# Kernel optimization log

Hardware: AMD Instinct MI355X
Metric: run time of the kernel (lower is better)

Reference implementation:

```python
import jax, jax.numpy as jnp
import numpy as np

B = 1024      # batchsz
T = 80        # max_review_len
E = 100       # embedding_len
U = 256       # units
V = 10000     # total_words


def _lstm_cell(x, c, h, wf, bf, wi, bi, wc, bc, wo, bo):
    # Faithful to LSTMlayer.call: four separate concat+matmul+bias gates.
    hx = jnp.concatenate([h, x], axis=1)          # [B, U + sec_dim]
    gf = jax.nn.sigmoid(hx @ wf + bf)             # forget gate
    gi = jax.nn.sigmoid(hx @ wi + bi)             # input gate (gr / wr1)
    ct = jnp.tanh(hx @ wc + bc)                   # candidate (wr2)
    c_new = gf * c + gi * ct
    go = jax.nn.sigmoid(hx @ wo + bo)             # output gate
    h_new = go * jnp.tanh(c_new)
    return c_new, h_new


def setup_inputs() -> dict:
    key = jax.random.key(0)
    ks = jax.random.split(key, 21)
    inp = {"tokens": jax.random.randint(ks[0], (B, T), 0, V, dtype=jnp.int32)}
    inp["emb"] = jax.random.normal(ks[1], (V, E), dtype=jnp.float32) * 0.1
    # Layer 1: sec_dim = E; Layer 2: sec_dim = U. stddev=0.1 matches init_weights.
    names = ["wf1", "wi1", "wc1", "wo1", "wf2", "wi2", "wc2", "wo2"]
    dims = [U + E] * 4 + [U + U] * 4
    for i, (n, d) in enumerate(zip(names, dims)):
        inp[n] = jax.random.normal(ks[2 + i], (d, U), dtype=jnp.float32) * 0.1
        inp["b" + n[1:]] = jnp.zeros((U,), dtype=jnp.float32)
    inp["w_out"] = jax.random.normal(ks[10], (U, 1), dtype=jnp.float32) * 0.1
    inp["b_out"] = jnp.zeros((1,), dtype=jnp.float32)
    return inp


def reference(tokens, emb, wf1, bf1, wi1, bi1, wc1, bc1, wo1, bo1,
              wf2, bf2, wi2, bi2, wc2, bc2, wo2, bo2, w_out, b_out):
    x = emb[tokens]                               # [B, T, E]
    init = (jnp.zeros((B, U), x.dtype), jnp.zeros((B, U), x.dtype),
            jnp.zeros((B, U), x.dtype), jnp.zeros((B, U), x.dtype))

    def step(carry, xt):
        c1, h1, c2, h2 = carry
        c1, h1 = _lstm_cell(xt, c1, h1, wf1, bf1, wi1, bi1, wc1, bc1, wo1, bo1)
        c2, h2 = _lstm_cell(h1, c2, h2, wf2, bf2, wi2, bi2, wc2, bc2, wo2, bo2)
        return (c1, h1, c2, h2), None

    carry, _ = jax.lax.scan(step, init, jnp.swapaxes(x, 0, 1))  # scan over T
    h2_last = carry[3]                            # [B, U]
    return jax.nn.sigmoid(h2_last @ w_out + b_out)  # [B, 1]
```

## Files before the change

### kernel.cpp

```cpp
#include <hip/hip_runtime.h>

typedef unsigned short u16;
typedef unsigned int uint;

using f32x4 = __attribute__((ext_vector_type(4))) float;
using bf16x8 = __attribute__((ext_vector_type(8))) __bf16;
using u32x4 = __attribute__((ext_vector_type(4))) uint;

static __device__ __forceinline__ bf16x8 as_bf16x8(uint4 u) {
    union { uint4 a; bf16x8 b; } c; c.a = u; return c.b;
}
static __device__ __forceinline__ bf16x8 as_bf16x8v(u32x4 u) {
    union { u32x4 a; bf16x8 b; } c; c.a = u; return c.b;
}
static __device__ __forceinline__ float bf2f(u16 h) {
    union { uint u; float f; } c; c.u = ((uint)h) << 16; return c.f;
}
static __device__ __forceinline__ u16 f2bf(float f) {
    union { float f; uint u; } c; c.f = f;
    uint u = c.u;
    return (u16)((u + 0x7fffu + ((u >> 16) & 1u)) >> 16);
}
static __device__ __forceinline__ float fast_sigmoid(float x) {
    x = fminf(30.f, fmaxf(-30.f, x));
    return __builtin_amdgcn_rcpf(1.0f + __builtin_amdgcn_exp2f(x * -1.44269504f));
}
static __device__ __forceinline__ float fast_tanh(float x) {
    x = fminf(15.f, fmaxf(-15.f, x));
    return 1.0f - 2.0f * __builtin_amdgcn_rcpf(1.0f + __builtin_amdgcn_exp2f(x * 2.88539008f));
}

static __device__ __forceinline__ u32x4 load_b128_sc0(const u16* p) {
    u32x4 r;
    asm volatile("global_load_dwordx4 %0, %1, off sc0" : "=v"(r) : "v"(p) : "memory");
    return r;
}
static __device__ __forceinline__ void wait_vm0_fence_sched() {
    asm volatile("s_waitcnt vmcnt(0)" ::: "memory");
    __builtin_amdgcn_sched_barrier(0);
}

static __device__ __forceinline__ float vext(f32x4 v, int i) {
    float r = v[0];
    r = (i == 1) ? v[1] : r;
    r = (i == 2) ? v[2] : r;
    r = (i == 3) ? v[3] : r;
    return r;
}
static __device__ __forceinline__ float sel4(float a0, float a1, float a2, float a3, int i) {
    float r = a0;
    r = (i == 1) ? a1 : r;
    r = (i == 2) ? a2 : r;
    r = (i == 3) ? a3 : r;
    return r;
}

static __device__ __forceinline__ int detect_fp32(const uint* w, int nwords) {
    int hits = 0;
    for (int i = 0; i < nwords; ++i) { uint e = (w[i] >> 7) & 0xffu; hits += (e >= 0x80u); }
    return hits > (nwords >> 3);
}
static __device__ __forceinline__ u16 load_bf(const void* p, int i, int fp32) {
    return fp32 ? f2bf(((const float*)p)[i]) : ((const u16*)p)[i];
}

__global__ void pack_w(const void* wf, const void* wi, const void* wc, const void* wo,
                       const void* bbf, const void* bbi, const void* bbc, const void* bbo,
                       u16* __restrict__ wp, u16* __restrict__ bp, int K, int KSTEPS) {
    __shared__ int sfp;
    if (threadIdx.x == 0) sfp = detect_fp32((const uint*)wf, 256);
    __syncthreads();
    const int fp32 = sfp;
    int w = blockIdx.x / KSTEPS, ks = blockIdx.x % KSTEPS;
    int nt = threadIdx.x >> 6, lane = threadIdx.x & 63;
    int c16 = lane & 15, q = lane >> 4;
    int n = w * 64 + nt * 16 + c16;
    int u = n >> 2, g = n & 3;
    const void* W = (g == 0) ? wf : (g == 1) ? wi : (g == 2) ? wc : wo;
    union { u16 v[8]; uint4 u4; } tmp;
#pragma unroll
    for (int j = 0; j < 8; ++j) {
        int k = ks * 32 + q * 8 + j;
        tmp.v[j] = (k < K) ? load_bf(W, k * 256 + u, fp32) : (u16)0;
    }
    *(uint4*)(wp + ((w * KSTEPS + ks) * 4 + nt) * 512 + lane * 8) = tmp.u4;
    if (ks == 0 && threadIdx.x < 64) {
        int n2 = w * 64 + threadIdx.x;
        int g2 = n2 & 3;
        const void* B = (g2 == 0) ? bbf : (g2 == 1) ? bbi : (g2 == 2) ? bbc : bbo;
        bp[n2] = load_bf(B, n2 >> 2, fp32);
    }
}

__global__ void pack_misc(const void* emb, const void* w_out, const void* b_out,
                          u16* __restrict__ embp, u16* __restrict__ wob,
                          u16* __restrict__ bob, uint* __restrict__ hzero) {
    __shared__ int sfp;
    if (threadIdx.x == 0) sfp = detect_fp32((const uint*)emb, 256);
    __syncthreads();
    const int fp32 = sfp;
    int gid = blockIdx.x * blockDim.x + threadIdx.x;
    int stride = gridDim.x * blockDim.x;
    for (int i = gid; i < 1000000; i += stride)
        embp[i] = load_bf(emb, i, fp32);
    for (int i = gid; i < 526336; i += stride) hzero[i] = 0;
    if (blockIdx.x == 0) {
        __shared__ int sfp2;
        if (threadIdx.x == 0) sfp2 = detect_fp32((const uint*)w_out, 128);
        __syncthreads();
        if (threadIdx.x < 256) wob[threadIdx.x] = load_bf(w_out, threadIdx.x, sfp2);
        if (threadIdx.x == 0) bob[0] = load_bf(b_out, 0, sfp2);
    }
}

static __device__ __forceinline__ void wv_wait(uint* grp, uint phase, int lane) {
    const uint* fp = grp + (lane & 15);
    uint* cnt = grp + 32;
    int k = 0;
    while (true) {
        uint v;
        asm volatile("global_load_dword %0, %1, off sc0\n\t"
                     "s_waitcnt vmcnt(0)"
                     : "=v"(v) : "v"(fp) : "memory");
        if (__all((int)(v >= phase))) break;
        if (((++k) & 7) == 0 &&
            __hip_atomic_load(cnt, __ATOMIC_RELAXED,
                              __HIP_MEMORY_SCOPE_AGENT) >= 16u * phase)
            break;
    }
}

static __device__ __forceinline__ void wv_arrive(uint* ldsc_ch, uint* grp, int g,
                                                 uint phase, int lane) {
    asm volatile("s_waitcnt vmcnt(0)" ::: "memory");
    if (lane == 0) {
        uint old = __hip_atomic_fetch_add(ldsc_ch, 1u, __ATOMIC_RELAXED,
                                          __HIP_MEMORY_SCOPE_WORKGROUP);
        if (old == 8u * phase - 1u) {
            uint* slot = grp + g;
            asm volatile("global_store_dword %0, %1, off sc0"
                         :: "v"(slot), "v"(phase) : "memory");
            __hip_atomic_fetch_add(grp + 32, 1u, __ATOMIC_RELAXED,
                                   __HIP_MEMORY_SCOPE_AGENT);
        }
    }
}

#define CSLAB 16384

__global__ void __launch_bounds__(1024, 1)
lstm_kernel(const int* __restrict__ tokens, const u16* __restrict__ embp,
            const u16* __restrict__ wp1, const u16* __restrict__ b1p,
            const u16* __restrict__ wp2, const u16* __restrict__ b2p,
            const u16* __restrict__ wob, const u16* __restrict__ bob,
            u16* __restrict__ h1g, u16* __restrict__ h2g,
            uint* __restrict__ flags, float* __restrict__ out) {
    __shared__ __align__(16) u16 w1s[12 * 4 * 512];
    __shared__ __align__(16) u16 w2s[16 * 4 * 512];
    __shared__ uint ldsc[2];
    __shared__ __align__(16) float outscr[1024];

    const int tid = threadIdx.x;
    const int bid = blockIdx.x;
    const int r2 = bid & 7;
    const int g = bid >> 3;
    const int lane = tid & 63;
    const int wv = tid >> 6;
    const int half = wv >> 3;
    const int w8 = wv & 7;
    const int nt = w8 & 3;
    const int mb = (w8 >> 2) * 2;
    const int c16 = lane & 15, q = lane >> 4;

    const int b = lane & 3;
    const int ulz = nt * 4 + ((lane & 15) >> 2);
    const int gunit = g * 16 + ulz;

    {
        const uint4* s1 = (const uint4*)(wp1 + g * (12 * 4 * 512));
        uint4* d1 = (uint4*)w1s;
        for (int i = tid; i < 3072; i += 1024) d1[i] = s1[i];
        const uint4* s2 = (const uint4*)(wp2 + g * (16 * 4 * 512));
        uint4* d2 = (uint4*)w2s;
        for (int i = tid; i < 4096; i += 1024) d2[i] = s2[i];
        if (tid < 2) ldsc[tid] = 0u;
    }
    ushort4 bl1 = *(const ushort4*)(b1p + gunit * 4);
    ushort4 bl2 = *(const ushort4*)(b2p + gunit * 4);
    const float b1f = bf2f(bl1.x), b1i = bf2f(bl1.y), b1c = bf2f(bl1.z), b1o = bf2f(bl1.w);
    const float b2f = bf2f(bl2.x), b2i = bf2f(bl2.y), b2c = bf2f(bl2.z), b2o = bf2f(bl2.w);
    float c1a = 0.f, c1b = 0.f, c2a = 0.f, c2b = 0.f;
    uint* fg = flags + (half * 8 + r2) * 64;
    uint* lc = &ldsc[half];
    __syncthreads();

    const u16* bp1 = w1s + nt * 512 + lane * 8;
    const u16* bp2 = w2s + nt * 512 + lane * 8;

    ushort4 xlo[4], xhi[4];
#define LOAD_X(m, t)                                                           \
    {                                                                          \
        int row = r2 * 128 + half * 64 + (m) * 16 + c16;                       \
        int tok = tokens[row * 80 + (t)];                                      \
        const u16* xb = embp + tok * 100 + q * 8;                              \
        _Pragma("unroll")                                                      \
        for (int k2 = 0; k2 < 4; ++k2) {                                       \
            xlo[k2] = *(const ushort4*)(xb + k2 * 32);                         \
            xhi[k2] = *(const ushort4*)(xb + k2 * 32 + 4);                     \
        }                                                                      \
    }
#define XFRAG(k2) ({ union { ushort4 a[2]; bf16x8 v; } xu;                     \
                     xu.a[0] = xlo[k2]; xu.a[1] = xhi[k2]; xu.v; })

#define GATES(accv, B0, B1, B2, B3, cref, hout)                                \
    {                                                                          \
        float v0 = vext(accv, b);                                              \
        float v1 = __shfl_xor(vext(accv, b ^ 1), 1, 64);                       \
        float v2 = __shfl_xor(vext(accv, b ^ 2), 2, 64);                       \
        float v3 = __shfl_xor(vext(accv, b ^ 3), 3, 64);                       \
        float zf = sel4(v0, v1, v2, v3, b);                                    \
        float zi = sel4(v0, v1, v2, v3, b ^ 1);                                \
        float zc = sel4(v0, v1, v2, v3, b ^ 2);                                \
        float zo = sel4(v0, v1, v2, v3, b ^ 3);                                \
        float gf = fast_sigmoid(zf + B0);                                      \
        float gi = fast_sigmoid(zi + B1);                                      \
        float gc = fast_tanh(zc + B2);                                         \
        float go = fast_sigmoid(zo + B3);                                      \
        float cn = gf * cref + gi * gc;                                        \
        cref = cn;                                                             \
        hout = f2bf(go * fast_tanh(cn));                                       \
    }

#define MSUB(m, acc1, c1ref, c2ref, p2r, p1r, p2w, p1w, iw)                    \
    {                                                                          \
        const int loffm = (q >> 1) * 1024 + ((m) * 16 + c16) * 16 + (q & 1) * 8; \
        const int hidxm = g * 1024 + ((m) * 16 + q * 4 + b) * 16 + ulz;        \
        const u16* h2b = h2g + (((p2r) * 2 + half) * 8 + r2) * CSLAB + loffm;  \
        const u16* h1b = h1g + (((p1r) * 2 + half) * 8 + r2) * CSLAB + loffm;  \
        u32x4 ag2[8], ag1[8];                                                  \
        _Pragma("unroll")                                                      \
        for (int ks = 0; ks < 8; ++ks) ag2[ks] = load_b128_sc0(h2b + ks * 2048); \
        _Pragma("unroll")                                                      \
        for (int ks = 0; ks < 8; ++ks) ag1[ks] = load_b128_sc0(h1b + ks * 2048); \
        wait_vm0_fence_sched();                                                \
        f32x4 acc2 = (f32x4){0.f, 0.f, 0.f, 0.f};                              \
        _Pragma("unroll")                                                      \
        for (int ks = 0; ks < 8; ++ks)                                         \
            acc2 = __builtin_amdgcn_mfma_f32_16x16x32_bf16(                    \
                as_bf16x8v(ag2[ks]), as_bf16x8(*(const uint4*)(bp2 + ks * 2048)), acc2, 0, 0, 0); \
        _Pragma("unroll")                                                      \
        for (int ks = 0; ks < 8; ++ks)                                         \
            acc2 = __builtin_amdgcn_mfma_f32_16x16x32_bf16(                    \
                as_bf16x8v(ag1[ks]), as_bf16x8(*(const uint4*)(bp2 + (8 + ks) * 2048)), acc2, 0, 0, 0); \
        _Pragma("unroll")                                                      \
        for (int ks = 0; ks < 8; ++ks)                                         \
            acc1 = __builtin_amdgcn_mfma_f32_16x16x32_bf16(                    \
                as_bf16x8v(ag1[ks]), as_bf16x8(*(const uint4*)(bp1 + ks * 2048)), acc1, 0, 0, 0); \
        u16 h2o, h1o;                                                          \
        GATES(acc2, b2f, b2i, b2c, b2o, c2ref, h2o);                           \
        GATES(acc1, b1f, b1i, b1c, b1o, c1ref, h1o);                           \
        h2g[(((p2w) * 2 + half) * 8 + r2) * CSLAB + hidxm] = h2o;              \
        h1g[(((p1w) * 2 + half) * 8 + r2) * CSLAB + hidxm] = h1o;              \
        (void)(iw);                                                            \
    }

    {
        LOAD_X(mb, 0);
        f32x4 acc = (f32x4){0.f, 0.f, 0.f, 0.f};
#pragma unroll
        for (int k2 = 0; k2 < 4; ++k2)
            acc = __builtin_amdgcn_mfma_f32_16x16x32_bf16(
                XFRAG(k2), as_bf16x8(*(const uint4*)(bp1 + (8 + k2) * 2048)), acc, 0, 0, 0);
        u16 h1o;
        GATES(acc, b1f, b1i, b1c, b1o, c1a, h1o);
        h1g[((0 * 2 + half) * 8 + r2) * CSLAB + g * 1024 + (mb * 16 + q * 4 + b) * 16 + ulz] = h1o;
        LOAD_X(mb + 1, 0);
        f32x4 accB = (f32x4){0.f, 0.f, 0.f, 0.f};
#pragma unroll
        for (int k2 = 0; k2 < 4; ++k2)
            accB = __builtin_amdgcn_mfma_f32_16x16x32_bf16(
                XFRAG(k2), as_bf16x8(*(const uint4*)(bp1 + (8 + k2) * 2048)), accB, 0, 0, 0);
        u16 h1oB;
        GATES(accB, b1f, b1i, b1c, b1o, c1b, h1oB);
        h1g[((0 * 2 + half) * 8 + r2) * CSLAB + g * 1024 + ((mb + 1) * 16 + q * 4 + b) * 16 + ulz] = h1oB;
        wv_arrive(lc, fg, g, 1u, lane);
    }

#pragma unroll 1
    for (int i = 0; i < 79; ++i) {
        const int p_h2r = (i + 1) & 1, p_h1r = i & 1;
        const int p_h2w = i & 1, p_h1w = (i + 1) & 1;

        LOAD_X(mb, i + 1);
        f32x4 acc1a = (f32x4){0.f, 0.f, 0.f, 0.f};
#pragma unroll
        for (int k2 = 0; k2 < 4; ++k2)
            acc1a = __builtin_amdgcn_mfma_f32_16x16x32_bf16(
                XFRAG(k2), as_bf16x8(*(const uint4*)(bp1 + (8 + k2) * 2048)), acc1a, 0, 0, 0);
        LOAD_X(mb + 1, i + 1);
        f32x4 acc1b = (f32x4){0.f, 0.f, 0.f, 0.f};
#pragma unroll
        for (int k2 = 0; k2 < 4; ++k2)
            acc1b = __builtin_amdgcn_mfma_f32_16x16x32_bf16(
                XFRAG(k2), as_bf16x8(*(const uint4*)(bp1 + (8 + k2) * 2048)), acc1b, 0, 0, 0);

        wv_wait(fg, (uint)(i + 1), lane);

        MSUB(mb, acc1a, c1a, c2a, p_h2r, p_h1r, p_h2w, p_h1w, i);
        MSUB(mb + 1, acc1b, c1b, c2b, p_h2r, p_h1r, p_h2w, p_h1w, i);

        wv_arrive(lc, fg, g, (uint)(i + 2), lane);
    }

    {
        wv_wait(fg, 80u, lane);
#pragma unroll 1
        for (int s = 0; s < 2; ++s) {
            const int m = mb + s;
            const int loffm = (q >> 1) * 1024 + (m * 16 + c16) * 16 + (q & 1) * 8;
            const int hidxm = g * 1024 + (m * 16 + q * 4 + b) * 16 + ulz;
            const u16* h2b = h2g + ((0 * 2 + half) * 8 + r2) * CSLAB + loffm;
            const u16* h1b = h1g + ((1 * 2 + half) * 8 + r2) * CSLAB + loffm;
            u32x4 ag2[8], ag1[8];
#pragma unroll
            for (int ks = 0; ks < 8; ++ks) ag2[ks] = load_b128_sc0(h2b + ks * 2048);
#pragma unroll
            for (int ks = 0; ks < 8; ++ks) ag1[ks] = load_b128_sc0(h1b + ks * 2048);
            wait_vm0_fence_sched();
            f32x4 acc2 = (f32x4){0.f, 0.f, 0.f, 0.f};
#pragma unroll
            for (int ks = 0; ks < 8; ++ks)
                acc2 = __builtin_amdgcn_mfma_f32_16x16x32_bf16(
                    as_bf16x8v(ag2[ks]), as_bf16x8(*(const uint4*)(bp2 + ks * 2048)), acc2, 0, 0, 0);
#pragma unroll
            for (int ks = 0; ks < 8; ++ks)
                acc2 = __builtin_amdgcn_mfma_f32_16x16x32_bf16(
                    as_bf16x8v(ag1[ks]), as_bf16x8(*(const uint4*)(bp2 + (8 + ks) * 2048)), acc2, 0, 0, 0);
            u16 h2o;
            if (s == 0) { GATES(acc2, b2f, b2i, b2c, b2o, c2a, h2o); }
            else        { GATES(acc2, b2f, b2i, b2c, b2o, c2b, h2o); }
            h2g[((1 * 2 + half) * 8 + r2) * CSLAB + hidxm] = h2o;
        }
        wv_arrive(lc, fg, g, 81u, lane);
        wv_wait(fg, 81u, lane);
    }
    __syncthreads();

    if (g == 0) {
#pragma unroll 1
        for (int ch = 0; ch < 2; ++ch) {
            const u16* base = h2g + ((1 * 2 + ch) * 8 + r2) * CSLAB;
            int rr = tid >> 4, s = tid & 15;
            const u16* hp = base + s * 1024 + rr * 16;
            u32x4 hv0 = load_b128_sc0(hp);
            u32x4 hv1 = load_b128_sc0(hp + 8);
            wait_vm0_fence_sched();
            const u16* wq = wob + s * 16;
            union { u32x4 v[2]; u16 h[16]; } hu; hu.v[0] = hv0; hu.v[1] = hv1;
            float dot = 0.f;
#pragma unroll
            for (int k = 0; k < 16; ++k) dot += bf2f(hu.h[k]) * bf2f(wq[k]);
            __syncthreads();
            outscr[rr * 16 + s] = dot;
            __syncthreads();
            if (tid < 64) {
                float ssum = 0.f;
                for (int k = 0; k < 16; ++k) ssum += outscr[tid * 16 + k];
                out[r2 * 128 + ch * 64 + tid] = fast_sigmoid(ssum + bf2f(bob[0]));
            }
        }
    }
}

extern "C" void kernel_launch(void* const* d_in, const int* in_sizes, int n_in,
                              void* d_out, int out_size, void* d_ws, size_t ws_size,
                              hipStream_t stream) {
    const int* tokens = (const int*)d_in[0];
    const void* emb = d_in[1];
    const void* wf1 = d_in[2];  const void* bf1_ = d_in[3];
    const void* wi1 = d_in[4];  const void* bi1_ = d_in[5];
    const void* wc1 = d_in[6];  const void* bc1_ = d_in[7];
    const void* wo1 = d_in[8];  const void* bo1_ = d_in[9];
    const void* wf2 = d_in[10]; const void* bf2_ = d_in[11];
    const void* wi2 = d_in[12]; const void* bi2_ = d_in[13];
    const void* wc2 = d_in[14]; const void* bc2_ = d_in[15];
    const void* wo2 = d_in[16]; const void* bo2_ = d_in[17];
    const void* w_out = d_in[18];
    const void* b_out = d_in[19];

    u16* wp1 = (u16*)d_ws;
    u16* wp2 = wp1 + 16 * 12 * 4 * 512;
    u16* b1p = wp2 + 16 * 16 * 4 * 512;
    u16* b2p = b1p + 1024;
    u16* wob = b2p + 1024;
    u16* bob = wob + 256;
    u16* embp = bob + 8;
    u16* h1g = embp + 1000000;
    u16* h2g = h1g + 524288;
    uint* flags = (uint*)(h2g + 524288);

    pack_w<<<dim3(16 * 12), dim3(256), 0, stream>>>(wf1, wi1, wc1, wo1, bf1_, bi1_, bc1_, bo1_,
                                                    wp1, b1p, 356, 12);
    pack_w<<<dim3(16 * 16), dim3(256), 0, stream>>>(wf2, wi2, wc2, wo2, bf2_, bi2_, bc2_, bo2_,
                                                    wp2, b2p, 512, 16);
    pack_misc<<<dim3(512), dim3(256), 0, stream>>>(emb, w_out, b_out, embp, wob, bob, (uint*)h1g);
    lstm_kernel<<<dim3(128), dim3(1024), 0, stream>>>(tokens, embp, wp1, b1p, wp2, b2p,
                                                      wob, bob, h1g, h2g, flags, (float*)d_out);
}
```

Baseline: 836.7 us.

## Split each block into four independent 32-row chains with packed h stores

```diff
diff --git a/kernel.cpp b/kernel.cpp
--- a/kernel.cpp
+++ b/kernel.cpp
@@ -123,7 +123,7 @@
                      "s_waitcnt vmcnt(0)"
                      : "=v"(v) : "v"(fp) : "memory");
         if (__all((int)(v >= phase))) break;
-        if (((++k) & 7) == 0 &&
+        if (((++k) & 31) == 0 &&
             __hip_atomic_load(cnt, __ATOMIC_RELAXED,
                               __HIP_MEMORY_SCOPE_AGENT) >= 16u * phase)
             break;
@@ -136,7 +136,7 @@
     if (lane == 0) {
         uint old = __hip_atomic_fetch_add(ldsc_ch, 1u, __ATOMIC_RELAXED,
                                           __HIP_MEMORY_SCOPE_WORKGROUP);
-        if (old == 8u * phase - 1u) {
+        if (old == 4u * phase - 1u) {
             uint* slot = grp + g;
             asm volatile("global_store_dword %0, %1, off sc0"
                          :: "v"(slot), "v"(phase) : "memory");
@@ -146,7 +146,7 @@
     }
 }
 
-#define CSLAB 16384
+#define CSLAB 8192
 
 __global__ void __launch_bounds__(1024, 1)
 lstm_kernel(const int* __restrict__ tokens, const u16* __restrict__ embp,
@@ -157,8 +157,8 @@
             uint* __restrict__ flags, float* __restrict__ out) {
     __shared__ __align__(16) u16 w1s[12 * 4 * 512];
     __shared__ __align__(16) u16 w2s[16 * 4 * 512];
-    __shared__ uint ldsc[2];
-    __shared__ __align__(16) float outscr[1024];
+    __shared__ uint ldsc[4];
+    __shared__ __align__(16) float outscr[512];
 
     const int tid = threadIdx.x;
     const int bid = blockIdx.x;
@@ -166,14 +166,13 @@
     const int g = bid >> 3;
     const int lane = tid & 63;
     const int wv = tid >> 6;
-    const int half = wv >> 3;
-    const int w8 = wv & 7;
-    const int nt = w8 & 3;
-    const int mb = (w8 >> 2) * 2;
+    const int ch = wv >> 2;
+    const int nt = wv & 3;
     const int c16 = lane & 15, q = lane >> 4;
 
     const int b = lane & 3;
-    const int ulz = nt * 4 + ((lane & 15) >> 2);
+    const int nib = (lane >> 2) & 3;
+    const int ulz = nt * 4 + nib;
     const int gunit = g * 16 + ulz;
 
     {
@@ -183,15 +182,15 @@
         const uint4* s2 = (const uint4*)(wp2 + g * (16 * 4 * 512));
         uint4* d2 = (uint4*)w2s;
         for (int i = tid; i < 4096; i += 1024) d2[i] = s2[i];
-        if (tid < 2) ldsc[tid] = 0u;
+        if (tid < 4) ldsc[tid] = 0u;
     }
     ushort4 bl1 = *(const ushort4*)(b1p + gunit * 4);
     ushort4 bl2 = *(const ushort4*)(b2p + gunit * 4);
     const float b1f = bf2f(bl1.x), b1i = bf2f(bl1.y), b1c = bf2f(bl1.z), b1o = bf2f(bl1.w);
     const float b2f = bf2f(bl2.x), b2i = bf2f(bl2.y), b2c = bf2f(bl2.z), b2o = bf2f(bl2.w);
     float c1a = 0.f, c1b = 0.f, c2a = 0.f, c2b = 0.f;
-    uint* fg = flags + (half * 8 + r2) * 64;
-    uint* lc = &ldsc[half];
+    uint* fg = flags + (ch * 8 + r2) * 64;
+    uint* lc = &ldsc[ch];
     __syncthreads();
 
     const u16* bp1 = w1s + nt * 512 + lane * 8;
@@ -200,7 +199,7 @@
     ushort4 xlo[4], xhi[4];
 #define LOAD_X(m, t)                                                           \
     {                                                                          \
-        int row = r2 * 128 + half * 64 + (m) * 16 + c16;                       \
+        int row = r2 * 128 + ch * 32 + (m) * 16 + c16;                         \
         int tok = tokens[row * 80 + (t)];                                      \
         const u16* xb = embp + tok * 100 + q * 8;                              \
         _Pragma("unroll")                                                      \
@@ -231,17 +230,29 @@
         hout = f2bf(go * fast_tanh(cn));                                       \
     }
 
-#define MSUB(m, acc1, c1ref, c2ref, p2r, p1r, p2w, p1w, iw)                    \
+#define STORE_H(hval, dstbase, m)                                              \
     {                                                                          \
-        const int loffm = (q >> 1) * 1024 + ((m) * 16 + c16) * 16 + (q & 1) * 8; \
-        const int hidxm = g * 1024 + ((m) * 16 + q * 4 + b) * 16 + ulz;        \
-        const u16* h2b = h2g + (((p2r) * 2 + half) * 8 + r2) * CSLAB + loffm;  \
-        const u16* h1b = h1g + (((p1r) * 2 + half) * 8 + r2) * CSLAB + loffm;  \
+        float hf = bf2f(hval);                                                 \
+        float p1 = __shfl_xor(hf, 4, 64);                                      \
+        float p2 = __shfl_xor(hf, 8, 64);                                      \
+        float p3 = __shfl_xor(hf, 12, 64);                                     \
+        if (nib == 0) {                                                        \
+            ushort4 pk;                                                        \
+            pk.x = hval; pk.y = f2bf(p1); pk.z = f2bf(p2); pk.w = f2bf(p3);    \
+            *(ushort4*)((dstbase) + g * 512 + ((m) * 16 + q * 4 + b) * 16 + nt * 4) = pk; \
+        }                                                                      \
+    }
+
+#define MSUB(m, acc1, c1ref, c2ref, p2r, p1r, p2w, p1w)                        \
+    {                                                                          \
+        const int loffm = (q >> 1) * 512 + ((m) * 16 + c16) * 16 + (q & 1) * 8; \
+        const u16* h2b = h2g + (((p2r) * 4 + ch) * 8 + r2) * CSLAB + loffm;    \
+        const u16* h1b = h1g + (((p1r) * 4 + ch) * 8 + r2) * CSLAB + loffm;    \
         u32x4 ag2[8], ag1[8];                                                  \
         _Pragma("unroll")                                                      \
-        for (int ks = 0; ks < 8; ++ks) ag2[ks] = load_b128_sc0(h2b + ks * 2048); \
-        _Pragma("unroll")                                                      \
-        for (int ks = 0; ks < 8; ++ks) ag1[ks] = load_b128_sc0(h1b + ks * 2048); \
+        for (int ks = 0; ks < 8; ++ks) ag2[ks] = load_b128_sc0(h2b + ks * 1024); \
+        _Pragma("unroll")                                                      \
+        for (int ks = 0; ks < 8; ++ks) ag1[ks] = load_b128_sc0(h1b + ks * 1024); \
         wait_vm0_fence_sched();                                                \
         f32x4 acc2 = (f32x4){0.f, 0.f, 0.f, 0.f};                              \
         _Pragma("unroll")                                                      \
@@ -259,13 +270,12 @@
         u16 h2o, h1o;                                                          \
         GATES(acc2, b2f, b2i, b2c, b2o, c2ref, h2o);                           \
         GATES(acc1, b1f, b1i, b1c, b1o, c1ref, h1o);                           \
-        h2g[(((p2w) * 2 + half) * 8 + r2) * CSLAB + hidxm] = h2o;              \
-        h1g[(((p1w) * 2 + half) * 8 + r2) * CSLAB + hidxm] = h1o;              \
-        (void)(iw);                                                            \
+        STORE_H(h2o, h2g + (((p2w) * 4 + ch) * 8 + r2) * CSLAB, m);            \
+        STORE_H(h1o, h1g + (((p1w) * 4 + ch) * 8 + r2) * CSLAB, m);            \
     }
 
     {
-        LOAD_X(mb, 0);
+        LOAD_X(0, 0);
         f32x4 acc = (f32x4){0.f, 0.f, 0.f, 0.f};
 #pragma unroll
         for (int k2 = 0; k2 < 4; ++k2)
@@ -273,8 +283,8 @@
                 XFRAG(k2), as_bf16x8(*(const uint4*)(bp1 + (8 + k2) * 2048)), acc, 0, 0, 0);
         u16 h1o;
         GATES(acc, b1f, b1i, b1c, b1o, c1a, h1o);
-        h1g[((0 * 2 + half) * 8 + r2) * CSLAB + g * 1024 + (mb * 16 + q * 4 + b) * 16 + ulz] = h1o;
-        LOAD_X(mb + 1, 0);
+        STORE_H(h1o, h1g + ((0 * 4 + ch) * 8 + r2) * CSLAB, 0);
+        LOAD_X(1, 0);
         f32x4 accB = (f32x4){0.f, 0.f, 0.f, 0.f};
 #pragma unroll
         for (int k2 = 0; k2 < 4; ++k2)
@@ -282,7 +292,7 @@
                 XFRAG(k2), as_bf16x8(*(const uint4*)(bp1 + (8 + k2) * 2048)), accB, 0, 0, 0);
         u16 h1oB;
         GATES(accB, b1f, b1i, b1c, b1o, c1b, h1oB);
-        h1g[((0 * 2 + half) * 8 + r2) * CSLAB + g * 1024 + ((mb + 1) * 16 + q * 4 + b) * 16 + ulz] = h1oB;
+        STORE_H(h1oB, h1g + ((0 * 4 + ch) * 8 + r2) * CSLAB, 1);
         wv_arrive(lc, fg, g, 1u, lane);
     }
 
@@ -291,13 +301,13 @@
         const int p_h2r = (i + 1) & 1, p_h1r = i & 1;
         const int p_h2w = i & 1, p_h1w = (i + 1) & 1;
 
-        LOAD_X(mb, i + 1);
+        LOAD_X(0, i + 1);
         f32x4 acc1a = (f32x4){0.f, 0.f, 0.f, 0.f};
 #pragma unroll
         for (int k2 = 0; k2 < 4; ++k2)
             acc1a = __builtin_amdgcn_mfma_f32_16x16x32_bf16(
                 XFRAG(k2), as_bf16x8(*(const uint4*)(bp1 + (8 + k2) * 2048)), acc1a, 0, 0, 0);
-        LOAD_X(mb + 1, i + 1);
+        LOAD_X(1, i + 1);
         f32x4 acc1b = (f32x4){0.f, 0.f, 0.f, 0.f};
 #pragma unroll
         for (int k2 = 0; k2 < 4; ++k2)
@@ -306,8 +316,8 @@
 
         wv_wait(fg, (uint)(i + 1), lane);
 
-        MSUB(mb, acc1a, c1a, c2a, p_h2r, p_h1r, p_h2w, p_h1w, i);
-        MSUB(mb + 1, acc1b, c1b, c2b, p_h2r, p_h1r, p_h2w, p_h1w, i);
+        MSUB(0, acc1a, c1a, c2a, p_h2r, p_h1r, p_h2w, p_h1w);
+        MSUB(1, acc1b, c1b, c2b, p_h2r, p_h1r, p_h2w, p_h1w);
 
         wv_arrive(lc, fg, g, (uint)(i + 2), lane);
     }
@@ -316,16 +326,15 @@
         wv_wait(fg, 80u, lane);
 #pragma unroll 1
         for (int s = 0; s < 2; ++s) {
-            const int m = mb + s;
-            const int loffm = (q >> 1) * 1024 + (m * 16 + c16) * 16 + (q & 1) * 8;
-            const int hidxm = g * 1024 + (m * 16 + q * 4 + b) * 16 + ulz;
-            const u16* h2b = h2g + ((0 * 2 + half) * 8 + r2) * CSLAB + loffm;
-            const u16* h1b = h1g + ((1 * 2 + half) * 8 + r2) * CSLAB + loffm;
+            const int m = s;
+            const int loffm = (q >> 1) * 512 + (m * 16 + c16) * 16 + (q & 1) * 8;
+            const u16* h2b = h2g + ((0 * 4 + ch) * 8 + r2) * CSLAB + loffm;
+            const u16* h1b = h1g + ((1 * 4 + ch) * 8 + r2) * CSLAB + loffm;
             u32x4 ag2[8], ag1[8];
 #pragma unroll
-            for (int ks = 0; ks < 8; ++ks) ag2[ks] = load_b128_sc0(h2b + ks * 2048);
-#pragma unroll
-            for (int ks = 0; ks < 8; ++ks) ag1[ks] = load_b128_sc0(h1b + ks * 2048);
+            for (int ks = 0; ks < 8; ++ks) ag2[ks] = load_b128_sc0(h2b + ks * 1024);
+#pragma unroll
+            for (int ks = 0; ks < 8; ++ks) ag1[ks] = load_b128_sc0(h1b + ks * 1024);
             wait_vm0_fence_sched();
             f32x4 acc2 = (f32x4){0.f, 0.f, 0.f, 0.f};
 #pragma unroll
@@ -339,7 +348,7 @@
             u16 h2o;
             if (s == 0) { GATES(acc2, b2f, b2i, b2c, b2o, c2a, h2o); }
             else        { GATES(acc2, b2f, b2i, b2c, b2o, c2b, h2o); }
-            h2g[((1 * 2 + half) * 8 + r2) * CSLAB + hidxm] = h2o;
+            STORE_H(h2o, h2g + ((1 * 4 + ch) * 8 + r2) * CSLAB, m);
         }
         wv_arrive(lc, fg, g, 81u, lane);
         wv_wait(fg, 81u, lane);
@@ -348,25 +357,27 @@
 
     if (g == 0) {
 #pragma unroll 1
-        for (int ch = 0; ch < 2; ++ch) {
-            const u16* base = h2g + ((1 * 2 + ch) * 8 + r2) * CSLAB;
+        for (int cc = 0; cc < 4; ++cc) {
+            const u16* base = h2g + ((1 * 4 + cc) * 8 + r2) * CSLAB;
             int rr = tid >> 4, s = tid & 15;
-            const u16* hp = base + s * 1024 + rr * 16;
-            u32x4 hv0 = load_b128_sc0(hp);
-            u32x4 hv1 = load_b128_sc0(hp + 8);
-            wait_vm0_fence_sched();
-            const u16* wq = wob + s * 16;
-            union { u32x4 v[2]; u16 h[16]; } hu; hu.v[0] = hv0; hu.v[1] = hv1;
             float dot = 0.f;
-#pragma unroll
-            for (int k = 0; k < 16; ++k) dot += bf2f(hu.h[k]) * bf2f(wq[k]);
+            if (tid < 512) {
+                const u16* hp = base + s * 512 + rr * 16;
+                u32x4 hv0 = load_b128_sc0(hp);
+                u32x4 hv1 = load_b128_sc0(hp + 8);
+                wait_vm0_fence_sched();
+                const u16* wq = wob + s * 16;
+                union { u32x4 v[2]; u16 h[16]; } hu; hu.v[0] = hv0; hu.v[1] = hv1;
+#pragma unroll
+                for (int k = 0; k < 16; ++k) dot += bf2f(hu.h[k]) * bf2f(wq[k]);
+            }
             __syncthreads();
-            outscr[rr * 16 + s] = dot;
+            if (tid < 512) outscr[rr * 16 + s] = dot;
             __syncthreads();
-            if (tid < 64) {
+            if (tid < 32) {
                 float ssum = 0.f;
                 for (int k = 0; k < 16; ++k) ssum += outscr[tid * 16 + k];
-                out[r2 * 128 + ch * 64 + tid] = fast_sigmoid(ssum + bf2f(bob[0]));
+                out[r2 * 128 + cc * 32 + tid] = fast_sigmoid(ssum + bf2f(bob[0]));
             }
         }
     }
```

After: 1.021 ms. +22.0%, slower.
